# Kernel tuning notes

Measured on AMD Instinct MI355X. Metric: run time of the kernel, lower is better.

Reference implementation:

```python
import jax, jax.numpy as jnp
import numpy as np
import math
from jax import lax

B, M, T = 32, 80, 10000
EPS = 1e-6
DELTA_CLAMP = (0.001, 0.1)


def setup_inputs() -> dict:
    key = jax.random.key(0)
    k_mel, = jax.random.split(key, 1)
    # linear mel energies: non-negative
    mel = jax.random.uniform(k_mel, (B, M, T), dtype=jnp.float32)

    def full(v):
        return jnp.full((M,), v, dtype=jnp.float32)

    # exact init values from the torch module
    log_s = full(math.log(0.15 / (1 - 0.15)))
    log_alpha = full(math.log(0.99 / (1 - 0.99)))
    log_delta = full(math.log(0.01))
    log_r = full(math.log(0.1 / (1 - 0.1)))
    return {"mel": mel, "log_s": log_s, "log_alpha": log_alpha,
            "log_delta": log_delta, "log_r": log_r}


def reference(mel, log_s, log_alpha, log_delta, log_r):
    # per-channel coefficients, clamped exactly as in torch
    s = jnp.clip(jax.nn.sigmoid(log_s), 0.05, 0.3)            # (M,)
    alpha = jnp.clip(jax.nn.sigmoid(log_alpha), 0.9, 0.999)   # (M,)
    delta = jnp.clip(jnp.exp(log_delta), *DELTA_CLAMP)        # (M,)
    r = jnp.clip(jax.nn.sigmoid(log_r), 0.05, 0.25)           # (M,)

    # EMA smoother along time via scan. Torch inits smoother = mel[:,:,0]
    # and the t=0 update yields (1-s)*mel0 + s*mel0 = mel0, so we scan over
    # all T frames with init = mel[:,:,0].
    s_bm = s[None, :]                      # (1, M) broadcasts over (B, M)

    def step(smoother, x_t):
        new = (1.0 - s_bm) * smoother + s_bm * x_t
        return new, new

    xs = jnp.moveaxis(mel, -1, 0)          # (T, B, M)
    _, sm = lax.scan(step, mel[:, :, 0], xs)
    smoothed = jnp.moveaxis(sm, 0, -1)     # (B, M, T)

    alpha_c = alpha[None, :, None]
    delta_c = delta[None, :, None]
    r_c = r[None, :, None]

    gain = (EPS + smoothed) ** (-alpha_c)
    pcen = (mel * gain + delta_c) ** r_c - delta_c ** r_c
    return pcen
```

## Files before the change

kernel.cpp:

```cpp
#include <hip/hip_runtime.h>
#include <math.h>


constexpr int B_ = 32, M_ = 80, T_ = 10000;
constexpr int EPI   = 512;
constexpr int CHUNK = 2048;
constexpr int NIT   = CHUNK / EPI;
constexpr int NCH   = (T_ + CHUNK - 1) / CHUNK;
constexpr float EPS_ = 1e-6f;

template <int CTRL, int ROWMASK, bool BC>
__device__ __forceinline__ float fdpp(float oldv, float v) {
    return __int_as_float(__builtin_amdgcn_update_dpp(
        __float_as_int(oldv), __float_as_int(v), CTRL, ROWMASK, 0xF, BC));
}
__device__ __forceinline__ float rdlane(float v, int l) {
    return __int_as_float(__builtin_amdgcn_readlane(__float_as_int(v), l));
}
__device__ __forceinline__ float fexp2(float x) { return __builtin_amdgcn_exp2f(x); }
__device__ __forceinline__ float flog2(float x) { return __builtin_amdgcn_logf(x); }

__global__ __launch_bounds__(256) void pcen_kernel(
    const float* __restrict__ mel,
    const float* __restrict__ log_s,
    const float* __restrict__ log_alpha,
    const float* __restrict__ log_delta,
    const float* __restrict__ log_r,
    float* __restrict__ out)
{
    const int lane = threadIdx.x & 63;
    const int wv   = threadIdx.x >> 6;
    const int gw   = blockIdx.x * 4 + wv;
    if (gw >= B_ * M_ * NCH) return;
    const int row = gw / NCH;
    const int c   = gw - row * NCH;
    const int m   = row % M_;

    const float* mp = mel + (size_t)row * T_;
    float*       op = out + (size_t)row * T_;
    const int start = c * CHUNK;

    float xh = 0.f;
    if (c > 0) xh = mp[start - 64 + lane];

    float4 xa[NIT], xb[NIT];
    bool   act[NIT];
    #pragma unroll
    for (int i = 0; i < NIT; ++i) {
        const int b = start + lane * 8 + i * EPI;
        act[i] = b < T_;
        xa[i] = make_float4(0, 0, 0, 0);
        xb[i] = xa[i];
        if (act[i]) { xa[i] = *(const float4*)(mp + b);
                      xb[i] = *(const float4*)(mp + b + 4); }
    }

    float s = 1.f / (1.f + __expf(-log_s[m]));         s = fminf(fmaxf(s, 0.05f), 0.3f);
    float alpha = 1.f / (1.f + __expf(-log_alpha[m])); alpha = fminf(fmaxf(alpha, 0.9f), 0.999f);
    float delta = __expf(log_delta[m]);                delta = fminf(fmaxf(delta, 0.001f), 0.1f);
    float r = 1.f / (1.f + __expf(-log_r[m]));         r = fminf(fmaxf(r, 0.05f), 0.25f);
    const float dr  = fexp2(r * flog2(delta));
    const float nal = -alpha;

    const float a   = 1.f - s;
    const float la2 = flog2(a);
    const float a2 = a*a, a3 = a2*a, a4 = a2*a2,
                a5 = a4*a, a6 = a4*a2, a7 = a4*a3, a8 = a4*a4;
    const float a16 = a8*a8, a32 = a16*a16;
    const float inv_a8 = 1.f / a8;
    const int   j16 = lane & 15;
    const float qlane  = fexp2(la2 * (float)(8 * (j16 + 1)));
    const float a8lane = fexp2(la2 * (float)(8 * lane));

    auto pcen1 = [&](float x, float y) {
        float g = fexp2(nal * flog2(y + EPS_));
        float z = fmaf(x, g, delta);
        return fexp2(r * flog2(z)) - dr;
    };

    auto iter = [&](const float4& va, const float4& vb, int bas, bool actv,
                    float ypv) -> float {
        float l0 = s * va.x;
        float l1 = fmaf(a, l0, s * va.y);
        float l2 = fmaf(a, l1, s * va.z);
        float l3 = fmaf(a, l2, s * va.w);
        float l4 = fmaf(a, l3, s * vb.x);
        float l5 = fmaf(a, l4, s * vb.y);
        float l6 = fmaf(a, l5, s * vb.z);
        float l7 = fmaf(a, l6, s * vb.w);

        float W = l7, t;
        t = fdpp<0x111, 0xF, true>(0.f, W);  W = fmaf(a8,  t, W);
        t = fdpp<0x112, 0xF, true>(0.f, W);  W = fmaf(a16, t, W);
        t = fdpp<0x114, 0xF, true>(0.f, W);  W = fmaf(a32, t, W);
        float Bv = fdpp<0x142, 0xE, false>(0.f, W);
        W = fmaf(qlane, Bv, W);

        float E = (W - l7) * inv_a8;
        float C = fmaf(a8lane, ypv, E);
        float ynext = rdlane(W, 63);

        if (actv) {
            float4 o1, o2;
            o1.x = pcen1(va.x, fmaf(a,  C, l0));
            o1.y = pcen1(va.y, fmaf(a2, C, l1));
            o1.z = pcen1(va.z, fmaf(a3, C, l2));
            o1.w = pcen1(va.w, fmaf(a4, C, l3));
            o2.x = pcen1(vb.x, fmaf(a5, C, l4));
            o2.y = pcen1(vb.y, fmaf(a6, C, l5));
            o2.z = pcen1(vb.z, fmaf(a7, C, l6));
            o2.w = pcen1(vb.w, fmaf(a8, C, l7));
            *(float4*)(op + bas)     = o1;
            *(float4*)(op + bas + 4) = o2;
        }
        return ynext;
    };

    float yprev;
    if (c == 0) {
        yprev = rdlane(xa[0].x, 0);
    } else {
        float u = s * xh * fexp2(la2 * (float)(63 - lane));
        u += __shfl_xor(u, 32);
        u += __shfl_xor(u, 16);
        u += __shfl_xor(u, 8);
        u += __shfl_xor(u, 4);
        u += __shfl_xor(u, 2);
        u += __shfl_xor(u, 1);
        yprev = u;
    }

    #pragma unroll
    for (int i = 0; i < NIT; ++i) {
        yprev = iter(xa[i], xb[i], start + lane * 8 + i * EPI, act[i], yprev);
    }
}

extern "C" void kernel_launch(void* const* d_in, const int* in_sizes, int n_in,
                              void* d_out, int out_size, void* d_ws, size_t ws_size,
                              hipStream_t stream) {
    const float* mel       = (const float*)d_in[0];
    const float* log_s     = (const float*)d_in[1];
    const float* log_alpha = (const float*)d_in[2];
    const float* log_delta = (const float*)d_in[3];
    const float* log_r     = (const float*)d_in[4];
    float* out = (float*)d_out;

    const int nwaves = B_ * M_ * NCH;
    dim3 grid((nwaves + 3) / 4);
    pcen_kernel<<<grid, 256, 0, stream>>>(mel, log_s, log_alpha, log_delta,
                                          log_r, out);
}
```

Before: 186.6 us.

## Switch to persistent waves processing contiguous chunk runs with prefetch and chained carries

The kernel now launches a fixed 8192 waves. Each wave walks a contiguous range of 1024-sample chunks, about 3.125 chunks per wave, and prefetches the next chunk's data while it computes the current one. When consecutive chunks sit in the same row, the running EMA carry is passed along instead of being rebuilt from a 64-sample warm-up reduction. The per-element smoothed values are now recomputed with a serial FMA chain rather than the a^k·C correction. Launch bounds are raised to aim for 8 blocks per CU. The risks are less parallelism per wave, an uneven number of chunks per wave, and longer serial dependency chains.

```diff
diff --git a/kernel.cpp b/kernel.cpp
--- a/kernel.cpp
+++ b/kernel.cpp
@@ -4,9 +4,10 @@
 
 constexpr int B_ = 32, M_ = 80, T_ = 10000;
 constexpr int EPI   = 512;
-constexpr int CHUNK = 2048;
-constexpr int NIT   = CHUNK / EPI;
-constexpr int NCH   = (T_ + CHUNK - 1) / CHUNK;
+constexpr int CHUNK = 1024;
+constexpr int NCH   = 10;
+constexpr int NT_   = B_ * M_ * NCH;
+constexpr int NW_   = 8192;
 constexpr float EPS_ = 1e-6f;
 
 template <int CTRL, int ROWMASK, bool BC>
@@ -20,7 +21,7 @@
 __device__ __forceinline__ float fexp2(float x) { return __builtin_amdgcn_exp2f(x); }
 __device__ __forceinline__ float flog2(float x) { return __builtin_amdgcn_logf(x); }
 
-__global__ __launch_bounds__(256) void pcen_kernel(
+__global__ __launch_bounds__(256, 8) void pcen_kernel(
     const float* __restrict__ mel,
     const float* __restrict__ log_s,
     const float* __restrict__ log_alpha,
@@ -31,46 +32,31 @@
     const int lane = threadIdx.x & 63;
     const int wv   = threadIdx.x >> 6;
     const int gw   = blockIdx.x * 4 + wv;
-    if (gw >= B_ * M_ * NCH) return;
-    const int row = gw / NCH;
-    const int c   = gw - row * NCH;
-    const int m   = row % M_;
+    if (gw >= NW_) return;
 
-    const float* mp = mel + (size_t)row * T_;
-    float*       op = out + (size_t)row * T_;
-    const int start = c * CHUNK;
+    const int lo = (gw * 25) >> 3;
+    const int hi = ((gw + 1) * 25) >> 3;
 
+    auto loadTask = [&](int t, float4& A0, float4& B0, float4& A1, float4& B1) {
+        const int row = t / NCH;
+        const int c   = t - row * NCH;
+        const int b   = c * CHUNK + lane * 8;
+        const float* p = mel + (size_t)row * T_ + b;
+        A0 = make_float4(0, 0, 0, 0); B0 = A0; A1 = A0; B1 = A0;
+        if (b < T_)       { A0 = *(const float4*)(p);       B0 = *(const float4*)(p + 4); }
+        if (b + EPI < T_) { A1 = *(const float4*)(p + EPI); B1 = *(const float4*)(p + EPI + 4); }
+    };
+
+    const int row0 = lo / NCH;
+    const int c0   = lo - row0 * NCH;
     float xh = 0.f;
-    if (c > 0) xh = mp[start - 64 + lane];
+    if (c0 > 0) xh = mel[(size_t)row0 * T_ + c0 * CHUNK - 64 + lane];
+    float4 ca0, cb0, ca1, cb1;
+    loadTask(lo, ca0, cb0, ca1, cb1);
 
-    float4 xa[NIT], xb[NIT];
-    bool   act[NIT];
-    #pragma unroll
-    for (int i = 0; i < NIT; ++i) {
-        const int b = start + lane * 8 + i * EPI;
-        act[i] = b < T_;
-        xa[i] = make_float4(0, 0, 0, 0);
-        xb[i] = xa[i];
-        if (act[i]) { xa[i] = *(const float4*)(mp + b);
-                      xb[i] = *(const float4*)(mp + b + 4); }
-    }
-
-    float s = 1.f / (1.f + __expf(-log_s[m]));         s = fminf(fmaxf(s, 0.05f), 0.3f);
-    float alpha = 1.f / (1.f + __expf(-log_alpha[m])); alpha = fminf(fmaxf(alpha, 0.9f), 0.999f);
-    float delta = __expf(log_delta[m]);                delta = fminf(fmaxf(delta, 0.001f), 0.1f);
-    float r = 1.f / (1.f + __expf(-log_r[m]));         r = fminf(fmaxf(r, 0.05f), 0.25f);
-    const float dr  = fexp2(r * flog2(delta));
-    const float nal = -alpha;
-
-    const float a   = 1.f - s;
-    const float la2 = flog2(a);
-    const float a2 = a*a, a3 = a2*a, a4 = a2*a2,
-                a5 = a4*a, a6 = a4*a2, a7 = a4*a3, a8 = a4*a4;
-    const float a16 = a8*a8, a32 = a16*a16;
-    const float inv_a8 = 1.f / a8;
-    const int   j16 = lane & 15;
-    const float qlane  = fexp2(la2 * (float)(8 * (j16 + 1)));
-    const float a8lane = fexp2(la2 * (float)(8 * lane));
+    float s, a, nal, delta, r, dr, la2;
+    float a8, a16, a32, inv_a8, qlane, a8lane;
+    const int j16 = lane & 15;
 
     auto pcen1 = [&](float x, float y) {
         float g = fexp2(nal * flog2(y + EPS_));
@@ -78,8 +64,8 @@
         return fexp2(r * flog2(z)) - dr;
     };
 
-    auto iter = [&](const float4& va, const float4& vb, int bas, bool actv,
-                    float ypv) -> float {
+    auto iter = [&](const float4& va, const float4& vb, float* op_, int bas,
+                    bool actv, float ypv) -> float {
         float l0 = s * va.x;
         float l1 = fmaf(a, l0, s * va.y);
         float l2 = fmaf(a, l1, s * va.z);
@@ -89,50 +75,87 @@
         float l6 = fmaf(a, l5, s * vb.z);
         float l7 = fmaf(a, l6, s * vb.w);
 
-        float W = l7, t;
-        t = fdpp<0x111, 0xF, true>(0.f, W);  W = fmaf(a8,  t, W);
-        t = fdpp<0x112, 0xF, true>(0.f, W);  W = fmaf(a16, t, W);
-        t = fdpp<0x114, 0xF, true>(0.f, W);  W = fmaf(a32, t, W);
+        float W = l7, tt;
+        tt = fdpp<0x111, 0xF, true>(0.f, W);  W = fmaf(a8,  tt, W);
+        tt = fdpp<0x112, 0xF, true>(0.f, W);  W = fmaf(a16, tt, W);
+        tt = fdpp<0x114, 0xF, true>(0.f, W);  W = fmaf(a32, tt, W);
         float Bv = fdpp<0x142, 0xE, false>(0.f, W);
         W = fmaf(qlane, Bv, W);
 
         float E = (W - l7) * inv_a8;
         float C = fmaf(a8lane, ypv, E);
-        float ynext = rdlane(W, 63);
+        float yn = rdlane(W, 63);
 
         if (actv) {
+            float y0 = fmaf(a, C,  l0);
+            float y1 = fmaf(a, y0, s * va.y);
+            float y2 = fmaf(a, y1, s * va.z);
+            float y3 = fmaf(a, y2, s * va.w);
+            float y4 = fmaf(a, y3, s * vb.x);
+            float y5 = fmaf(a, y4, s * vb.y);
+            float y6 = fmaf(a, y5, s * vb.z);
+            float y7 = fmaf(a, y6, s * vb.w);
             float4 o1, o2;
-            o1.x = pcen1(va.x, fmaf(a,  C, l0));
-            o1.y = pcen1(va.y, fmaf(a2, C, l1));
-            o1.z = pcen1(va.z, fmaf(a3, C, l2));
-            o1.w = pcen1(va.w, fmaf(a4, C, l3));
-            o2.x = pcen1(vb.x, fmaf(a5, C, l4));
-            o2.y = pcen1(vb.y, fmaf(a6, C, l5));
-            o2.z = pcen1(vb.z, fmaf(a7, C, l6));
-            o2.w = pcen1(vb.w, fmaf(a8, C, l7));
-            *(float4*)(op + bas)     = o1;
-            *(float4*)(op + bas + 4) = o2;
+            o1.x = pcen1(va.x, y0);
+            o1.y = pcen1(va.y, y1);
+            o1.z = pcen1(va.z, y2);
+            o1.w = pcen1(va.w, y3);
+            o2.x = pcen1(vb.x, y4);
+            o2.y = pcen1(vb.y, y5);
+            o2.z = pcen1(vb.z, y6);
+            o2.w = pcen1(vb.w, y7);
+            *(float4*)(op_ + bas)     = o1;
+            *(float4*)(op_ + bas + 4) = o2;
         }
-        return ynext;
+        return yn;
     };
 
-    float yprev;
-    if (c == 0) {
-        yprev = rdlane(xa[0].x, 0);
-    } else {
-        float u = s * xh * fexp2(la2 * (float)(63 - lane));
-        u += __shfl_xor(u, 32);
-        u += __shfl_xor(u, 16);
-        u += __shfl_xor(u, 8);
-        u += __shfl_xor(u, 4);
-        u += __shfl_xor(u, 2);
-        u += __shfl_xor(u, 1);
-        yprev = u;
-    }
+    float yprev = 0.f;
+    bool chained = false;
+    for (int t = lo; t < hi; ++t) {
+        float4 na0, nb0, na1, nb1;
+        const bool more = (t + 1) < hi;
+        if (more) loadTask(t + 1, na0, nb0, na1, nb1);
 
-    #pragma unroll
-    for (int i = 0; i < NIT; ++i) {
-        yprev = iter(xa[i], xb[i], start + lane * 8 + i * EPI, act[i], yprev);
+        const int row = t / NCH;
+        const int c   = t - row * NCH;
+        const int m   = row % M_;
+
+        s = 1.f / (1.f + __expf(-log_s[m]));         s = fminf(fmaxf(s, 0.05f), 0.3f);
+        float alpha = 1.f / (1.f + __expf(-log_alpha[m]));
+        alpha = fminf(fmaxf(alpha, 0.9f), 0.999f);
+        nal = -alpha;
+        delta = __expf(log_delta[m]);                delta = fminf(fmaxf(delta, 0.001f), 0.1f);
+        r = 1.f / (1.f + __expf(-log_r[m]));         r = fminf(fmaxf(r, 0.05f), 0.25f);
+        dr  = fexp2(r * flog2(delta));
+        a   = 1.f - s;
+        la2 = flog2(a);
+        float a2 = a * a, a4 = a2 * a2;
+        a8  = a4 * a4; a16 = a8 * a8; a32 = a16 * a16;
+        inv_a8 = 1.f / a8;
+        qlane  = fexp2(la2 * (float)(8 * (j16 + 1)));
+        a8lane = fexp2(la2 * (float)(8 * lane));
+
+        if (c == 0) {
+            yprev = rdlane(ca0.x, 0);
+        } else if (!chained) {
+            float u = s * xh * fexp2(la2 * (float)(63 - lane));
+            u += __shfl_xor(u, 32);
+            u += __shfl_xor(u, 16);
+            u += __shfl_xor(u, 8);
+            u += __shfl_xor(u, 4);
+            u += __shfl_xor(u, 2);
+            u += __shfl_xor(u, 1);
+            yprev = u;
+        }
+
+        float* op_ = out + (size_t)row * T_;
+        const int base = c * CHUNK + lane * 8;
+        yprev = iter(ca0, cb0, op_, base,       base < T_,       yprev);
+        yprev = iter(ca1, cb1, op_, base + EPI, base + EPI < T_, yprev);
+        chained = true;
+
+        ca0 = na0; cb0 = nb0; ca1 = na1; cb1 = nb1;
     }
 }
 
@@ -146,8 +169,7 @@
     const float* log_r     = (const float*)d_in[4];
     float* out = (float*)d_out;
 
-    const int nwaves = B_ * M_ * NCH;
-    dim3 grid((nwaves + 3) / 4);
+    dim3 grid(NW_ / 4);
     pcen_kernel<<<grid, 256, 0, stream>>>(mel, log_s, log_alpha, log_delta,
                                           log_r, out);
 }
```

New measurement: 200.7 us. 1.08x slower.
